# Kernel tuning notes

Measured on AMD Instinct MI355X. Metric: run time of the kernel, lower is better.

## Reference

```python
import jax, jax.numpy as jnp
import numpy as np

# raster settings (match init_kwargs)
H, W = 512, 512
TANFOVX, TANFOVY = 0.5, 0.5
DENSITY_SHIFT = -2.0
SCALE_MOD = 1.0
SH_DEG = 2
N, R, D = 262144, 8, 8

SH_C0 = 0.28209479177387814
SH_C1 = 0.4886025119029199
SH_C2 = (1.0925484305920792, -1.0925484305920792, 0.31539156525252005,
         -1.0925484305920792, 0.5462742152960396)


def _camera():
    # row-vector convention: p_view = p_world @ V[:3,:3] + V[3,:3]
    view = np.eye(4, dtype=np.float32)
    view[3, 2] = 3.0  # camera at (0,0,-3) looking down +z
    znear, zfar = 0.01, 100.0
    top, right = TANFOVY * znear, TANFOVX * znear
    P = np.zeros((4, 4), np.float32)
    P[0, 0] = znear / right
    P[1, 1] = znear / top
    P[2, 2] = zfar / (zfar - znear)
    P[2, 3] = 1.0
    P[3, 2] = -zfar * znear / (zfar - znear)
    proj = view @ P  # full world->clip, row-vector convention
    campos = np.array([0.0, 0.0, -3.0], np.float32)
    return jnp.asarray(view), jnp.asarray(proj), jnp.asarray(campos)


def setup_inputs() -> dict:
    key = jax.random.key(0)
    ks = jax.random.split(key, 6)
    positions = jax.random.uniform(ks[0], (N, 3), jnp.float32)          # local coords in [0,1]
    trivecs = jax.random.normal(ks[1], (N, R, 3, D), jnp.float32)
    densities = jax.random.normal(ks[2], (N, R), jnp.float32)
    shs = jax.random.normal(ks[3], (N, R, (SH_DEG + 1) ** 2, 3), jnp.float32) * 0.3
    view, proj, campos = _camera()
    aabb = jnp.array([-1.0, -1.0, -1.0, 2.0, 2.0, 2.0], jnp.float32)    # [origin, size]
    bg = jnp.zeros((3,), jnp.float32)
    rnd = jnp.full((H, W, 3), 0.5, jnp.float32)
    rnd = rnd.at[..., 2].set(jax.random.uniform(ks[4], (H, W), jnp.float32))
    return {"positions": positions, "trivecs": trivecs, "densities": densities,
            "shs": shs, "viewmatrix": view, "projmatrix": proj, "campos": campos,
            "aabb": aabb, "bg": bg, "random_image": rnd}


def _rasterize(positions, trivecs, densities, shs, viewmatrix, projmatrix, campos, aabb, bg):
    world = aabb[:3] + positions * aabb[3:]                              # [N,3]
    ones = jnp.ones((world.shape[0], 1), world.dtype)
    ph = jnp.concatenate([world, ones], 1) @ projmatrix                  # [N,4]
    ndc = ph[:, :3] / (ph[:, 3:4] + 1e-7)
    pview = world @ viewmatrix[:3, :3] + viewmatrix[3, :3]
    depth = pview[:, 2]                                                  # [N]
    ix = jnp.round(((ndc[:, 0] + 1.0) * W - 1.0) * 0.5).astype(jnp.int32)
    iy = jnp.round(((ndc[:, 1] + 1.0) * H - 1.0) * 0.5).astype(jnp.int32)
    valid = (depth > 0.2) & (ix >= 0) & (ix < W) & (iy >= 0) & (iy < H)
    pid = jnp.where(valid, iy * W + ix, H * W)                           # dump bucket H*W

    # trivec density at the cell center: product of the three axis vectors
    mid = trivecs[:, :, :, D // 2]                                       # [N,R,3]
    tri = jax.nn.relu(jnp.prod(mid, axis=-1))                            # [N,R]
    sigma_r = jnp.exp(densities + DENSITY_SHIFT) * tri * SCALE_MOD       # [N,R]
    sigma = sigma_r.sum(-1)
    alpha = jnp.clip(1.0 - jnp.exp(-sigma), 0.0, 0.999)                  # [N]

    # per-rank SH color, density-weighted over ranks
    dirs = world - campos
    dirs = dirs / (jnp.linalg.norm(dirs, axis=-1, keepdims=True) + 1e-8)
    x, y, z = dirs[:, 0:1], dirs[:, 1:2], dirs[:, 2:3]
    basis = jnp.concatenate([
        jnp.full_like(x, SH_C0),
        -SH_C1 * y, SH_C1 * z, -SH_C1 * x,
        SH_C2[0] * x * y, SH_C2[1] * y * z,
        SH_C2[2] * (2.0 * z * z - x * x - y * y),
        SH_C2[3] * x * z, SH_C2[4] * (x * x - y * y)], axis=1)           # [N,9]
    color_r = jnp.maximum(jnp.einsum('nk,nrkc->nrc', basis, shs) + 0.5, 0.0)
    wr = sigma_r / (sigma + 1e-8)[:, None]
    color = jnp.einsum('nr,nrc->nc', wr, color_r)                        # [N,3]

    # depth-sorted per-pixel alpha compositing via segmented exclusive cumsum
    order = jnp.lexsort((depth, pid))
    pid_s, a_s = pid[order], alpha[order]
    c_s, d_s = color[order], depth[order]
    logs = jnp.log1p(-a_s)
    excl = jnp.cumsum(logs) - logs                                       # exclusive cumsum
    first = jnp.searchsorted(pid_s, pid_s, side='left')                  # segment start idx
    T = jnp.exp(excl - excl[first])                                      # transmittance
    wgt = a_s * T
    npx = H * W
    img_c = jax.ops.segment_sum(wgt[:, None] * c_s, pid_s, num_segments=npx + 1)[:npx]
    img_a = jax.ops.segment_sum(wgt, pid_s, num_segments=npx + 1)[:npx]
    img_d = jax.ops.segment_sum(wgt * d_s, pid_s, num_segments=npx + 1)[:npx]
    img_c = img_c + (1.0 - img_a)[:, None] * bg
    pct_d = img_d / (img_a + 1e-8)
    return (img_c.reshape(H, W, 3).transpose(2, 0, 1),
            img_d.reshape(H, W), img_a.reshape(H, W), pct_d.reshape(H, W))


def reference(positions, trivecs, densities, shs, viewmatrix, projmatrix, campos, aabb, bg, random_image):
    # random_image is only used for stochastic jitter in the CUDA kernel; deterministic here
    return _rasterize(positions, trivecs, densities, shs, viewmatrix, projmatrix, campos, aabb, bg)
```

## Files before the change

### kernel.cpp

```cpp
#include <hip/hip_runtime.h>
#include <math.h>
#include <float.h>

#define Hh 512
#define Ww 512
#define HWW (Hh*Ww)
#define NP 262144
#define RR 8
#define KMAX 32


__global__ __launch_bounds__(256) void point_kernel(
    const float* __restrict__ positions,
    const float* __restrict__ trivecs,
    const float* __restrict__ densities,
    const float* __restrict__ shs,
    const float* __restrict__ viewm,
    const float* __restrict__ projm,
    const float* __restrict__ campos,
    const float* __restrict__ aabb,
    float* __restrict__ recs,
    int* __restrict__ heads)
{
#pragma clang fp contract(off)
    int gid = blockIdx.x * blockDim.x + threadIdx.x;
    int n    = gid >> 1;
    int half = gid & 1;

    float px = positions[n*3+0], py = positions[n*3+1], pz = positions[n*3+2];
    float wx = aabb[0] + px*aabb[3];
    float wy = aabb[1] + py*aabb[4];
    float wz = aabb[2] + pz*aabb[5];

    float phx = ((wx*projm[0] + wy*projm[4]) + wz*projm[8])  + projm[12];
    float phy = ((wx*projm[1] + wy*projm[5]) + wz*projm[9])  + projm[13];
    float phw = ((wx*projm[3] + wy*projm[7]) + wz*projm[11]) + projm[15];
    float denom = phw + 1e-7f;
    float ndcx = phx / denom;
    float ndcy = phy / denom;
    float depth = ((wx*viewm[2] + wy*viewm[6]) + wz*viewm[10]) + viewm[14];

    float fx = ((ndcx + 1.0f)*(float)Ww - 1.0f)*0.5f;
    float fy = ((ndcy + 1.0f)*(float)Hh - 1.0f)*0.5f;
    int ix = (int)rintf(fx);
    int iy = (int)rintf(fy);
    bool valid = (depth > 0.2f) && (ix >= 0) && (ix < Ww) && (iy >= 0) && (iy < Hh);
    int pid = valid ? (iy*Ww + ix) : -1;

    float4 d = *(const float4*)(densities + (size_t)n*RR + half*4);
    float den[4] = {d.x, d.y, d.z, d.w};
    const float* tv = trivecs + (size_t)n*RR*24 + half*4*24;
    float sr[4]; float sig_half = 0.0f;
    #pragma unroll
    for (int r = 0; r < 4; r++){
        float m0 = tv[r*24 + 4];
        float m1 = tv[r*24 + 12];
        float m2 = tv[r*24 + 20];
        float tri = m0*m1*m2;
        tri = tri > 0.0f ? tri : 0.0f;
        float s = expf(den[r] - 2.0f) * tri;
        sr[r] = s; sig_half += s;
    }
    float sigma = sig_half + __shfl_xor(sig_half, 1, 64);
    float alpha = 1.0f - expf(-sigma);
    alpha = fminf(alpha, 0.999f);
    alpha = fmaxf(alpha, 0.0f);

    float dxr = wx - campos[0], dyr = wy - campos[1], dzr = wz - campos[2];
    float nrm = sqrtf((dxr*dxr + dyr*dyr) + dzr*dzr) + 1e-8f;
    float x = dxr/nrm, y = dyr/nrm, z = dzr/nrm;
    float basis[9];
    basis[0] = 0.28209479177387814f;
    basis[1] = -0.4886025119029199f * y;
    basis[2] =  0.4886025119029199f * z;
    basis[3] = -0.4886025119029199f * x;
    basis[4] =  1.0925484305920792f * (x*y);
    basis[5] = -1.0925484305920792f * (y*z);
    basis[6] =  0.31539156525252005f * (2.0f*z*z - x*x - y*y);
    basis[7] = -1.0925484305920792f * (x*z);
    basis[8] =  0.5462742152960396f * (x*x - y*y);

    float dot[4][3];
    #pragma unroll
    for (int r = 0; r < 4; r++){ dot[r][0]=0.f; dot[r][1]=0.f; dot[r][2]=0.f; }
    const float4* sp = (const float4*)(shs + (size_t)n*(RR*27)) + half*27;
    #pragma unroll
    for (int j = 0; j < 27; j++){
        float4 v = sp[j];
        float e[4] = {v.x, v.y, v.z, v.w};
        #pragma unroll
        for (int q = 0; q < 4; q++){
            int f = 4*j + q;
            int r = f / 27;
            int k = (f % 27) / 3;
            int c = f % 3;
            dot[r][c] = fmaf(basis[k], e[q], dot[r][c]);
        }
    }
    float invs = 1.0f/(sigma + 1e-8f);
    float cr = 0.f, cg = 0.f, cb = 0.f;
    #pragma unroll
    for (int r = 0; r < 4; r++){
        float wr = sr[r]*invs;
        cr = fmaf(wr, fmaxf(dot[r][0] + 0.5f, 0.0f), cr);
        cg = fmaf(wr, fmaxf(dot[r][1] + 0.5f, 0.0f), cg);
        cb = fmaf(wr, fmaxf(dot[r][2] + 0.5f, 0.0f), cb);
    }
    cr += __shfl_xor(cr, 1, 64);
    cg += __shfl_xor(cg, 1, 64);
    cb += __shfl_xor(cb, 1, 64);

    if (half == 0 && pid >= 0){
        int next = atomicExch(&heads[pid], n);
        float4* rp = (float4*)(recs + (size_t)n*8);
        rp[0] = make_float4(depth, alpha, cr, cg);
        rp[1] = make_float4(cb, __int_as_float(next), 0.0f, 0.0f);
    }
}

__global__ __launch_bounds__(256) void composite_kernel(
    const int* __restrict__ heads,
    const float* __restrict__ recs,
    const float* __restrict__ bg,
    float* __restrict__ out)
{
    int p = blockIdx.x * blockDim.x + threadIdx.x;
    if (p >= HWW) return;

    unsigned long long keys[KMAX];
    int cnt = 0;
    int cur = heads[p];
    while (cur >= 0){
        float dpt = recs[(size_t)cur*8 + 0];
        int  nxt  = __float_as_int(recs[(size_t)cur*8 + 5]);
        if (cnt < KMAX)
            keys[cnt] = ((unsigned long long)__float_as_uint(dpt) << 32) |
                        (unsigned int)cur;
        cnt++;
        cur = nxt;
    }

    float T = 1.0f, accA = 0.f, accD = 0.f, aR = 0.f, aG = 0.f, aB = 0.f;

    if (cnt <= KMAX){
        for (int i = 1; i < cnt; i++){
            unsigned long long k = keys[i];
            int j = i - 1;
            while (j >= 0 && keys[j] > k){ keys[j+1] = keys[j]; j--; }
            keys[j+1] = k;
        }
        for (int i = 0; i < cnt; i++){
            int nidx = (int)(keys[i] & 0xffffffffu);
            float4 ra = *(const float4*)(recs + (size_t)nidx*8);
            float4 rb = *(const float4*)(recs + (size_t)nidx*8 + 4);
            float a = ra.y, w = a*T;
            aR += w*ra.z; aG += w*ra.w; aB += w*rb.x;
            accA += w; accD += w*ra.x;
            T *= (1.0f - a);
        }
    } else {
        unsigned long long last = 0; bool haveLast = false;
        for (int it = 0; it < cnt; ++it){
            unsigned long long best = ~0ull; int bn = -1;
            for (int c2 = heads[p]; c2 >= 0; ){
                float dpt = recs[(size_t)c2*8 + 0];
                int  nxt  = __float_as_int(recs[(size_t)c2*8 + 5]);
                unsigned long long k =
                    ((unsigned long long)__float_as_uint(dpt) << 32) |
                    (unsigned int)c2;
                if ((!haveLast || k > last) && k < best){ best = k; bn = c2; }
                c2 = nxt;
            }
            float4 ra = *(const float4*)(recs + (size_t)bn*8);
            float4 rb = *(const float4*)(recs + (size_t)bn*8 + 4);
            float a = ra.y, w = a*T;
            aR += w*ra.z; aG += w*ra.w; aB += w*rb.x;
            accA += w; accD += w*ra.x;
            T *= (1.0f - a);
            last = best; haveLast = true;
        }
    }

    float om = 1.0f - accA;
    out[p]         = aR + om*bg[0];
    out[HWW + p]   = aG + om*bg[1];
    out[2*HWW + p] = aB + om*bg[2];
    out[3*HWW + p] = accD;
    out[4*HWW + p] = accA;
    out[5*HWW + p] = accD/(accA + 1e-8f);
}

extern "C" void kernel_launch(void* const* d_in, const int* in_sizes, int n_in,
                              void* d_out, int out_size, void* d_ws, size_t ws_size,
                              hipStream_t stream)
{
    const float* positions = (const float*)d_in[0];
    const float* trivecs   = (const float*)d_in[1];
    const float* densities = (const float*)d_in[2];
    const float* shs       = (const float*)d_in[3];
    const float* viewm     = (const float*)d_in[4];
    const float* projm     = (const float*)d_in[5];
    const float* campos    = (const float*)d_in[6];
    const float* aabb      = (const float*)d_in[7];
    const float* bg        = (const float*)d_in[8];
    float* out = (float*)d_out;

    char* ws = (char*)d_ws;
    size_t o = 0;
    int*   heads = (int*)(ws + o);   o += (size_t)HWW*4;
    float* recs  = (float*)(ws + o); o += (size_t)NP*32;

    hipMemsetAsync(heads, 0xFF, (size_t)HWW*4, stream);
    point_kernel<<<(NP*2)/256, 256, 0, stream>>>(positions, trivecs, densities, shs,
                                                 viewm, projm, campos, aabb,
                                                 recs, heads);
    composite_kernel<<<HWW/256, 256, 0, stream>>>(heads, recs, bg, out);
}
```

Baseline: 510.2 us.

## Hoist point loads, pack depth/next in records, register-only selection sort compositing

The point kernel now issues all density, trivec and SH loads up front to raise memory-level parallelism. The record layout places depth and next pointer together, so list traversal reads one float2 instead of two scattered scalars. Compositing gathers up to 16 keys into registers with a fully unrolled fixed-length walk. It then repeatedly extracts the minimum with a tree reduction and exits early through a wave-wide any check, replacing the dynamically indexed insertion sort that likely spilled to scratch. The costs are higher register pressure from holding 27 float4 SH values per thread, and a smaller KMAX, so more pixels may take the slow overflow path.

```diff
diff --git a/kernel.cpp b/kernel.cpp
--- a/kernel.cpp
+++ b/kernel.cpp
@@ -6,9 +6,13 @@
 #define Ww 512
 #define HWW (Hh*Ww)
 #define NP 262144
-#define RR 8
-#define KMAX 32
-
+#define KMAX 16
+
+
+__device__ __forceinline__ unsigned long long umin64(unsigned long long a,
+                                                     unsigned long long b){
+    return a < b ? a : b;
+}
 
 __global__ __launch_bounds__(256) void point_kernel(
     const float* __restrict__ positions,
@@ -28,6 +32,23 @@
     int half = gid & 1;
 
     float px = positions[n*3+0], py = positions[n*3+1], pz = positions[n*3+2];
+
+    float4 dv = *(const float4*)(densities + (size_t)n*8 + half*4);
+
+    const float* tv = trivecs + (size_t)n*192 + half*96;
+    float tvm[12];
+    #pragma unroll
+    for (int r = 0; r < 4; r++){
+        tvm[r*3+0] = tv[r*24 + 4];
+        tvm[r*3+1] = tv[r*24 + 12];
+        tvm[r*3+2] = tv[r*24 + 20];
+    }
+
+    const float4* sp = (const float4*)(shs + (size_t)n*216) + half*27;
+    float4 sh[27];
+    #pragma unroll
+    for (int j = 0; j < 27; j++) sh[j] = sp[j];
+
     float wx = aabb[0] + px*aabb[3];
     float wy = aabb[1] + py*aabb[4];
     float wz = aabb[2] + pz*aabb[5];
@@ -47,16 +68,11 @@
     bool valid = (depth > 0.2f) && (ix >= 0) && (ix < Ww) && (iy >= 0) && (iy < Hh);
     int pid = valid ? (iy*Ww + ix) : -1;
 
-    float4 d = *(const float4*)(densities + (size_t)n*RR + half*4);
-    float den[4] = {d.x, d.y, d.z, d.w};
-    const float* tv = trivecs + (size_t)n*RR*24 + half*4*24;
+    float den[4] = {dv.x, dv.y, dv.z, dv.w};
     float sr[4]; float sig_half = 0.0f;
     #pragma unroll
     for (int r = 0; r < 4; r++){
-        float m0 = tv[r*24 + 4];
-        float m1 = tv[r*24 + 12];
-        float m2 = tv[r*24 + 20];
-        float tri = m0*m1*m2;
+        float tri = tvm[r*3+0]*tvm[r*3+1]*tvm[r*3+2];
         tri = tri > 0.0f ? tri : 0.0f;
         float s = expf(den[r] - 2.0f) * tri;
         sr[r] = s; sig_half += s;
@@ -83,11 +99,9 @@
     float dot[4][3];
     #pragma unroll
     for (int r = 0; r < 4; r++){ dot[r][0]=0.f; dot[r][1]=0.f; dot[r][2]=0.f; }
-    const float4* sp = (const float4*)(shs + (size_t)n*(RR*27)) + half*27;
     #pragma unroll
     for (int j = 0; j < 27; j++){
-        float4 v = sp[j];
-        float e[4] = {v.x, v.y, v.z, v.w};
+        float e[4] = {sh[j].x, sh[j].y, sh[j].z, sh[j].w};
         #pragma unroll
         for (int q = 0; q < 4; q++){
             int f = 4*j + q;
@@ -113,8 +127,8 @@
     if (half == 0 && pid >= 0){
         int next = atomicExch(&heads[pid], n);
         float4* rp = (float4*)(recs + (size_t)n*8);
-        rp[0] = make_float4(depth, alpha, cr, cg);
-        rp[1] = make_float4(cb, __int_as_float(next), 0.0f, 0.0f);
+        rp[0] = make_float4(depth, __int_as_float(next), alpha, cr);
+        *(float2*)(recs + (size_t)n*8 + 4) = make_float2(cg, cb);
     }
 }
 
@@ -127,54 +141,73 @@
     int p = blockIdx.x * blockDim.x + threadIdx.x;
     if (p >= HWW) return;
 
+    const unsigned long long NONE = ~0ull;
     unsigned long long keys[KMAX];
-    int cnt = 0;
     int cur = heads[p];
-    while (cur >= 0){
-        float dpt = recs[(size_t)cur*8 + 0];
-        int  nxt  = __float_as_int(recs[(size_t)cur*8 + 5]);
-        if (cnt < KMAX)
-            keys[cnt] = ((unsigned long long)__float_as_uint(dpt) << 32) |
-                        (unsigned int)cur;
-        cnt++;
-        cur = nxt;
-    }
+
+    #pragma unroll
+    for (int i = 0; i < KMAX; i++){
+        unsigned long long k = NONE;
+        if (cur >= 0){
+            float2 dn = *(const float2*)(recs + (size_t)cur*8);
+            k = ((unsigned long long)__float_as_uint(dn.x) << 32) |
+                (unsigned int)cur;
+            cur = __float_as_int(dn.y);
+        }
+        keys[i] = k;
+    }
+    bool overflow = (cur >= 0);
 
     float T = 1.0f, accA = 0.f, accD = 0.f, aR = 0.f, aG = 0.f, aB = 0.f;
 
-    if (cnt <= KMAX){
-        for (int i = 1; i < cnt; i++){
-            unsigned long long k = keys[i];
-            int j = i - 1;
-            while (j >= 0 && keys[j] > k){ keys[j+1] = keys[j]; j--; }
-            keys[j+1] = k;
-        }
-        for (int i = 0; i < cnt; i++){
-            int nidx = (int)(keys[i] & 0xffffffffu);
-            float4 ra = *(const float4*)(recs + (size_t)nidx*8);
-            float4 rb = *(const float4*)(recs + (size_t)nidx*8 + 4);
-            float a = ra.y, w = a*T;
-            aR += w*ra.z; aG += w*ra.w; aB += w*rb.x;
-            accA += w; accD += w*ra.x;
-            T *= (1.0f - a);
+    if (!overflow){
+        for (int it = 0; it < KMAX; ++it){
+            unsigned long long m0 = umin64(keys[0],  keys[1]);
+            unsigned long long m1 = umin64(keys[2],  keys[3]);
+            unsigned long long m2 = umin64(keys[4],  keys[5]);
+            unsigned long long m3 = umin64(keys[6],  keys[7]);
+            unsigned long long m4 = umin64(keys[8],  keys[9]);
+            unsigned long long m5 = umin64(keys[10], keys[11]);
+            unsigned long long m6 = umin64(keys[12], keys[13]);
+            unsigned long long m7 = umin64(keys[14], keys[15]);
+            m0 = umin64(m0, m1); m2 = umin64(m2, m3);
+            m4 = umin64(m4, m5); m6 = umin64(m6, m7);
+            m0 = umin64(m0, m2); m4 = umin64(m4, m6);
+            unsigned long long m = umin64(m0, m4);
+
+            if (!__any(m != NONE)) break;
+
+            if (m != NONE){
+                int nidx = (int)(m & 0xffffffffu);
+                float4 ra = *(const float4*)(recs + (size_t)nidx*8);
+                float2 rb = *(const float2*)(recs + (size_t)nidx*8 + 4);
+                float a = ra.z, w = a*T;
+                aR += w*ra.w; aG += w*rb.x; aB += w*rb.y;
+                accA += w; accD += w*ra.x;
+                T *= (1.0f - a);
+                #pragma unroll
+                for (int j = 0; j < KMAX; j++)
+                    keys[j] = (keys[j] == m) ? NONE : keys[j];
+            }
         }
     } else {
         unsigned long long last = 0; bool haveLast = false;
-        for (int it = 0; it < cnt; ++it){
-            unsigned long long best = ~0ull; int bn = -1;
+        for (;;){
+            unsigned long long best = NONE;
             for (int c2 = heads[p]; c2 >= 0; ){
-                float dpt = recs[(size_t)c2*8 + 0];
-                int  nxt  = __float_as_int(recs[(size_t)c2*8 + 5]);
+                float2 dn = *(const float2*)(recs + (size_t)c2*8);
                 unsigned long long k =
-                    ((unsigned long long)__float_as_uint(dpt) << 32) |
+                    ((unsigned long long)__float_as_uint(dn.x) << 32) |
                     (unsigned int)c2;
-                if ((!haveLast || k > last) && k < best){ best = k; bn = c2; }
-                c2 = nxt;
+                if ((!haveLast || k > last) && k < best) best = k;
+                c2 = __float_as_int(dn.y);
             }
-            float4 ra = *(const float4*)(recs + (size_t)bn*8);
-            float4 rb = *(const float4*)(recs + (size_t)bn*8 + 4);
-            float a = ra.y, w = a*T;
-            aR += w*ra.z; aG += w*ra.w; aB += w*rb.x;
+            if (best == NONE) break;
+            int nidx = (int)(best & 0xffffffffu);
+            float4 ra = *(const float4*)(recs + (size_t)nidx*8);
+            float2 rb = *(const float2*)(recs + (size_t)nidx*8 + 4);
+            float a = ra.z, w = a*T;
+            aR += w*ra.w; aG += w*rb.x; aB += w*rb.y;
             accA += w; accD += w*ra.x;
             T *= (1.0f - a);
             last = best; haveLast = true;
```

New measurement: 501.0 us. Within noise of the previous version (-1.8%).
